# Optimization experiments

Hardware: AMD Instinct MI355X
Metric: run time of the kernel (lower is better)

Reference implementation:

```python
import jax, jax.numpy as jnp
import numpy as np

B, C, F, H = 16384, 64, 128, 128  # batch, conv1d_out_channel, in_features, hidden


def setup_inputs() -> dict:
    key = jax.random.key(0)
    k_x, k_w1, k_w2 = jax.random.split(key, 3)
    inputline = jax.random.normal(k_x, (B, C, F), dtype=jnp.float32)
    # Per-channel cloned Flowconf MLP params: Linear(F,H) -> ReLU -> Linear(H,1)
    W1 = jax.random.normal(k_w1, (C, F, H), dtype=jnp.float32) * (1.0 / np.sqrt(F))
    b1 = jnp.zeros((C, H), dtype=jnp.float32)
    W2 = jax.random.normal(k_w2, (C, H), dtype=jnp.float32) * (1.0 / np.sqrt(H))
    b2 = jnp.zeros((C,), dtype=jnp.float32)
    return {"inputline": inputline, "W1": W1, "b1": b1, "W2": W2, "b2": b2}


def reference(inputline, W1, b1, W2, b2) -> jnp.ndarray:
    # Batched over channels: replaces the Python loop over C cloned submodules
    # with indexed assignment into output[:, i].
    h = jax.nn.relu(jnp.einsum("bcf,cfh->bch", inputline, W1) + b1)  # [B,C,H]
    out = jnp.einsum("bch,ch->bc", h, W2) + b2                        # [B,C]
    return out.sum(axis=-1)                                           # [B]
```

## Files before the change

### kernel.cpp

```cpp
#include <hip/hip_runtime.h>
#include <hip/hip_bf16.h>

#define B_TOT 16384
#define C_CH  64
#define F_IN  128
#define H_HID 128
#define ROWS  512

using f32x4  = __attribute__((ext_vector_type(4))) float;
using bf16x8 = __attribute__((ext_vector_type(8))) short;

__device__ inline unsigned pack2(float a, float b) {
    unsigned short lo = __builtin_bit_cast(unsigned short, __float2bfloat16(a));
    unsigned short hi = __builtin_bit_cast(unsigned short, __float2bfloat16(b));
    return (unsigned)lo | ((unsigned)hi << 16);
}

__device__ inline void load_sub(const float* __restrict__ X, int rbase, int c,
                                int l15, int lg, float4 (&r)[8]) {
    const float* xb = X + ((size_t)(rbase + l15) * C_CH + c) * F_IN + lg * 8;
    #pragma unroll
    for (int ks = 0; ks < 4; ++ks) {
        r[ks * 2]     = *reinterpret_cast<const float4*>(xb + ks * 32);
        r[ks * 2 + 1] = *reinterpret_cast<const float4*>(xb + ks * 32 + 4);
    }
}

__device__ inline void compute_sub(const char* ws, const float4 (&r)[8],
                                   const float (&w2v)[8], const float (&b1v)[8],
                                   float b2c, int rbase, int l15, int lg,
                                   float* __restrict__ out)
{
    f32x4 acc[8];
    #pragma unroll
    for (int nf = 0; nf < 8; ++nf) acc[nf] = f32x4{0.f, 0.f, 0.f, 0.f};

    #pragma unroll
    for (int ks = 0; ks < 4; ++ks) {
        const int kbyte = ks * 64 + lg * 16;
        float4 r0 = r[ks * 2], r1 = r[ks * 2 + 1];
        uint4 pa;
        pa.x = pack2(r0.x, r0.y);
        pa.y = pack2(r0.z, r0.w);
        pa.z = pack2(r1.x, r1.y);
        pa.w = pack2(r1.z, r1.w);
        bf16x8 a = __builtin_bit_cast(bf16x8, pa);
        #pragma unroll
        for (int nf = 0; nf < 8; ++nf) {
            int n = nf * 16 + l15;
            bf16x8 b = *reinterpret_cast<const bf16x8*>(
                ws + n * 256 + (kbyte ^ ((n & 7) << 4)));
            acc[nf] = __builtin_amdgcn_mfma_f32_16x16x32_bf16(a, b, acc[nf], 0, 0, 0);
        }
    }

    float part[4] = {0.f, 0.f, 0.f, 0.f};
    #pragma unroll
    for (int nf = 0; nf < 8; ++nf)
        #pragma unroll
        for (int j = 0; j < 4; ++j)
            part[j] += fmaxf(acc[nf][j] + b1v[nf], 0.f) * w2v[nf];
    #pragma unroll
    for (int off = 8; off >= 1; off >>= 1)
        #pragma unroll
        for (int j = 0; j < 4; ++j)
            part[j] += __shfl_xor(part[j], off, 64);
    if (l15 == 0) {
        int row = rbase + lg * 4;
        #pragma unroll
        for (int j = 0; j < 4; ++j)
            atomicAdd(&out[row + j], part[j] + b2c);
    }
}

__global__ __launch_bounds__(256, 2)
void fused_mlp_kernel(const float* __restrict__ X,
                      const float* __restrict__ W1,
                      const float* __restrict__ b1,
                      const float* __restrict__ W2,
                      const float* __restrict__ b2,
                      float* __restrict__ out)
{
    __shared__ short Ws[H_HID * F_IN];

    const int t    = threadIdx.x;
    const int lane = t & 63;
    const int wave = t >> 6;
    const int c    = blockIdx.x;
    const int m0   = blockIdx.y * ROWS;

    char* ws = reinterpret_cast<char*>(Ws);

    {
        const int n  = t & 127;
        const int kh = (t >> 7) * 64;
        const float* wbase = W1 + (size_t)c * F_IN * H_HID + n;
        #pragma unroll
        for (int kk = 0; kk < 64; kk += 8) {
            float f[8];
            #pragma unroll
            for (int j = 0; j < 8; ++j)
                f[j] = wbase[(size_t)(kh + kk + j) * H_HID];
            uint4 p;
            p.x = pack2(f[0], f[1]);
            p.y = pack2(f[2], f[3]);
            p.z = pack2(f[4], f[5]);
            p.w = pack2(f[6], f[7]);
            int byte = ((kh + kk) * 2) ^ ((n & 7) << 4);
            *reinterpret_cast<uint4*>(ws + n * 256 + byte) = p;
        }
    }

    const int l15 = lane & 15;
    const int lg  = lane >> 4;

    float w2v[8], b1v[8];
    #pragma unroll
    for (int nf = 0; nf < 8; ++nf) {
        w2v[nf] = W2[c * H_HID + nf * 16 + l15];
        b1v[nf] = b1[c * H_HID + nf * 16 + l15];
    }
    const float b2c = b2[c];

    __syncthreads();

    float4 rA[8], rB[8];
    load_sub(X, m0 + wave * 16, c, l15, lg, rA);

    #pragma unroll 1
    for (int sc = 0; sc < 8; sc += 2) {
        const int rbA = m0 + (sc * 4 + wave) * 16;
        const int rbB = m0 + ((sc + 1) * 4 + wave) * 16;
        load_sub(X, rbB, c, l15, lg, rB);
        compute_sub(ws, rA, w2v, b1v, b2c, rbA, l15, lg, out);
        if (sc + 2 < 8)
            load_sub(X, m0 + ((sc + 2) * 4 + wave) * 16, c, l15, lg, rA);
        compute_sub(ws, rB, w2v, b1v, b2c, rbB, l15, lg, out);
    }
}

extern "C" void kernel_launch(void* const* d_in, const int* in_sizes, int n_in,
                              void* d_out, int out_size, void* d_ws, size_t ws_size,
                              hipStream_t stream) {
    const float* X  = (const float*)d_in[0];
    const float* W1 = (const float*)d_in[1];
    const float* b1 = (const float*)d_in[2];
    const float* W2 = (const float*)d_in[3];
    const float* b2 = (const float*)d_in[4];
    float* out = (float*)d_out;

    hipMemsetAsync(out, 0, (size_t)out_size * sizeof(float), stream);

    dim3 grid(C_CH, B_TOT / ROWS);
    fused_mlp_kernel<<<grid, dim3(256), 0, stream>>>(X, W1, b1, W2, b2, out);
}
```

Baseline: 118.5 us.

## Stream X tiles directly into LDS with per-wave triple buffering

X tiles are now loaded with global_load_lds into a per-wave triple buffer in shared memory instead of registers, and hand-placed vmcnt waits keep three tiles in flight while the current one is computed. Each block covers twice as many rows, which spreads the W1 conversion over more work. Per-row results are gathered with shuffles so 16 lanes each issue one atomic, replacing 4 atomics per lane on a quarter of the lanes. The larger shared-memory footprint (about 128KB) likely allows only one block per CU, and the vmcnt counts depend on the exact number of outstanding memory operations.

```diff
diff --git a/kernel.cpp b/kernel.cpp
--- a/kernel.cpp
+++ b/kernel.cpp
@@ -5,7 +5,8 @@
 #define C_CH  64
 #define F_IN  128
 #define H_HID 128
-#define ROWS  512
+#define ROWS  1024
+#define NSUB  16
 
 using f32x4  = __attribute__((ext_vector_type(4))) float;
 using bf16x8 = __attribute__((ext_vector_type(8))) short;
@@ -16,35 +17,44 @@
     return (unsigned)lo | ((unsigned)hi << 16);
 }
 
-__device__ inline void load_sub(const float* __restrict__ X, int rbase, int c,
-                                int l15, int lg, float4 (&r)[8]) {
-    const float* xb = X + ((size_t)(rbase + l15) * C_CH + c) * F_IN + lg * 8;
-    #pragma unroll
-    for (int ks = 0; ks < 4; ++ks) {
-        r[ks * 2]     = *reinterpret_cast<const float4*>(xb + ks * 32);
-        r[ks * 2 + 1] = *reinterpret_cast<const float4*>(xb + ks * 32 + 4);
-    }
+__device__ inline void gld_lds16(const float* g, float* l) {
+    __builtin_amdgcn_global_load_lds(
+        (const __attribute__((address_space(1))) void*)g,
+        (__attribute__((address_space(3))) void*)l, 16, 0, 0);
 }
 
-__device__ inline void compute_sub(const char* ws, const float4 (&r)[8],
-                                   const float (&w2v)[8], const float (&b1v)[8],
-                                   float b2c, int rbase, int l15, int lg,
-                                   float* __restrict__ out)
+__device__ inline void issue_tile(const float* __restrict__ X, int rbase, int c,
+                                  int lane, float* xbuf) {
+    const float* g = X + ((size_t)(rbase + (lane & 15)) * C_CH + c) * F_IN
+                       + (lane >> 4) * 4;
+    #pragma unroll
+    for (int j = 0; j < 8; ++j)
+        gld_lds16(g + j * 16, xbuf + j * 256);
+}
+
+template<int N>
+__device__ inline float compute_round(const float* __restrict__ xb, const char* ws,
+                                      const float (&w2v)[8], const float (&b1v)[8],
+                                      int lane, int l15, int lg)
 {
+    asm volatile("s_waitcnt vmcnt(%0)" :: "i"(N) : "memory");
+
     f32x4 acc[8];
     #pragma unroll
     for (int nf = 0; nf < 8; ++nf) acc[nf] = f32x4{0.f, 0.f, 0.f, 0.f};
 
     #pragma unroll
     for (int ks = 0; ks < 4; ++ks) {
-        const int kbyte = ks * 64 + lg * 16;
-        float4 r0 = r[ks * 2], r1 = r[ks * 2 + 1];
+        const int o = ks * 512 + (lg >> 1) * 256 + (lg & 1) * 128 + l15 * 4;
+        float4 r0 = *reinterpret_cast<const float4*>(xb + o);
+        float4 r1 = *reinterpret_cast<const float4*>(xb + o + 64);
         uint4 pa;
         pa.x = pack2(r0.x, r0.y);
         pa.y = pack2(r0.z, r0.w);
         pa.z = pack2(r1.x, r1.y);
         pa.w = pack2(r1.z, r1.w);
         bf16x8 a = __builtin_bit_cast(bf16x8, pa);
+        const int kbyte = ks * 64 + lg * 16;
         #pragma unroll
         for (int nf = 0; nf < 8; ++nf) {
             int n = nf * 16 + l15;
@@ -65,12 +75,13 @@
         #pragma unroll
         for (int j = 0; j < 4; ++j)
             part[j] += __shfl_xor(part[j], off, 64);
-    if (l15 == 0) {
-        int row = rbase + lg * 4;
-        #pragma unroll
-        for (int j = 0; j < 4; ++j)
-            atomicAdd(&out[row + j], part[j] + b2c);
-    }
+    int src = (lane & 12) << 2;
+    float v0 = __shfl(part[0], src, 64);
+    float v1 = __shfl(part[1], src, 64);
+    float v2 = __shfl(part[2], src, 64);
+    float v3 = __shfl(part[3], src, 64);
+    int s = lane & 3;
+    return (s == 0) ? v0 : (s == 1) ? v1 : (s == 2) ? v2 : v3;
 }
 
 __global__ __launch_bounds__(256, 2)
@@ -81,15 +92,24 @@
                       const float* __restrict__ b2,
                       float* __restrict__ out)
 {
-    __shared__ short Ws[H_HID * F_IN];
+    __shared__ alignas(16) short Ws[H_HID * F_IN];
+    __shared__ alignas(16) float Xs[4 * 3 * 2048];
 
     const int t    = threadIdx.x;
     const int lane = t & 63;
     const int wave = t >> 6;
     const int c    = blockIdx.x;
     const int m0   = blockIdx.y * ROWS;
+    const int l15  = lane & 15;
+    const int lg   = lane >> 4;
 
-    char* ws = reinterpret_cast<char*>(Ws);
+    char*  ws    = reinterpret_cast<char*>(Ws);
+    float* slice = &Xs[wave * 3 * 2048];
+    float *bu0 = slice, *bu1 = slice + 2048, *bu2 = slice + 4096;
+
+    issue_tile(X, m0 + (0 * 4 + wave) * 16, c, lane, bu0);
+    issue_tile(X, m0 + (1 * 4 + wave) * 16, c, lane, bu1);
+    issue_tile(X, m0 + (2 * 4 + wave) * 16, c, lane, bu2);
 
     {
         const int n  = t & 127;
@@ -111,9 +131,6 @@
         }
     }
 
-    const int l15 = lane & 15;
-    const int lg  = lane >> 4;
-
     float w2v[8], b1v[8];
     #pragma unroll
     for (int nf = 0; nf < 8; ++nf) {
@@ -124,18 +141,30 @@
 
     __syncthreads();
 
-    float4 rA[8], rB[8];
-    load_sub(X, m0 + wave * 16, c, l15, lg, rA);
-
     #pragma unroll 1
-    for (int sc = 0; sc < 8; sc += 2) {
-        const int rbA = m0 + (sc * 4 + wave) * 16;
-        const int rbB = m0 + ((sc + 1) * 4 + wave) * 16;
-        load_sub(X, rbB, c, l15, lg, rB);
-        compute_sub(ws, rA, w2v, b1v, b2c, rbA, l15, lg, out);
-        if (sc + 2 < 8)
-            load_sub(X, m0 + ((sc + 2) * 4 + wave) * 16, c, l15, lg, rA);
-        compute_sub(ws, rB, w2v, b1v, b2c, rbB, l15, lg, out);
+    for (int sc = 0; sc < NSUB - 3; ++sc) {
+        const int rbase = m0 + (sc * 4 + wave) * 16;
+        float val = compute_round<17>(bu0, ws, w2v, b1v, lane, l15, lg);
+        issue_tile(X, m0 + ((sc + 3) * 4 + wave) * 16, c, lane, bu0);
+        if (lane < 16) atomicAdd(&out[rbase + lane], val + b2c);
+        float* tmp = bu0; bu0 = bu1; bu1 = bu2; bu2 = tmp;
+    }
+    {
+        const int rbase = m0 + (13 * 4 + wave) * 16;
+        float val = compute_round<17>(bu0, ws, w2v, b1v, lane, l15, lg);
+        if (lane < 16) atomicAdd(&out[rbase + lane], val + b2c);
+        float* tmp = bu0; bu0 = bu1; bu1 = bu2; bu2 = tmp;
+    }
+    {
+        const int rbase = m0 + (14 * 4 + wave) * 16;
+        float val = compute_round<9>(bu0, ws, w2v, b1v, lane, l15, lg);
+        if (lane < 16) atomicAdd(&out[rbase + lane], val + b2c);
+        float* tmp = bu0; bu0 = bu1; bu1 = bu2; bu2 = tmp;
+    }
+    {
+        const int rbase = m0 + (15 * 4 + wave) * 16;
+        float val = compute_round<1>(bu0, ws, w2v, b1v, lane, l15, lg);
+        if (lane < 16) atomicAdd(&out[rbase + lane], val + b2c);
     }
 }
 
```

After: 130.0 us. 9.8% more time.
